# Performance work log

Hardware: AMD Instinct MI355X
Metric: run time of the kernel (lower is better)

The kernel has to match this reference:

```python
import jax, jax.numpy as jnp
import numpy as np

ALPHA = 1.0
GAMMA = 0.8
TAU = 0.1
NUM_SAMPLES = 10
TOP_K = 100
NUM_USER_GROUPS = 8
NUM_ITEM_GROUPS = 16
BATCH = 1024
NUM_ITEMS = 10000


def setup_inputs() -> dict:
    key = jax.random.key(0)
    k1, k2, k3, k4 = jax.random.split(key, 4)
    pred_scores = jax.random.normal(k1, (BATCH, NUM_ITEMS), dtype=jnp.float32)
    true_scores = jax.random.uniform(k2, (BATCH, NUM_ITEMS), dtype=jnp.float32)
    user_groups = jax.random.randint(k3, (BATCH,), 0, NUM_USER_GROUPS)
    item_groups = jax.random.randint(k4, (NUM_ITEMS,), 0, NUM_ITEM_GROUPS)
    return {
        "pred_scores": pred_scores,
        "true_scores": true_scores,
        "user_groups": user_groups,
        "item_groups": item_groups,
    }


def _calculate_exposure(scores):
    # scores: [B, k]. Soft-rank via Gumbel perturbations + pairwise sigmoid.
    B, k = scores.shape
    noise = jax.random.gumbel(jax.random.key(1), (NUM_SAMPLES, B, k), dtype=scores.dtype)
    noisy = scores[None, :, :] + noise                       # [S, B, k]
    diffs = noisy[..., :, None] - noisy[..., None, :]        # [S, B, k, k]
    # ranks = 1 + sum_j sigmoid((s_i - s_j)/tau) - sigmoid(0)
    ranks = 1.0 + jax.nn.sigmoid(diffs / TAU).sum(axis=-1) - 0.5  # [S, B, k]
    exposure = jnp.power(GAMMA, ranks - 1.0)                 # [S, B, k]
    return exposure.mean(axis=0)                             # [B, k]


def reference(pred_scores, true_scores, user_groups, item_groups):
    B = pred_scores.shape[0]
    # top-k selection (values == gathered pred scores)
    pred_topk, topk_idx = jax.lax.top_k(pred_scores, TOP_K)   # [B, k]
    item_groups_topk = item_groups[topk_idx]                  # [B, k]

    system_exposure = _calculate_exposure(pred_topk)          # [B, k]
    target_exposure = jnp.full_like(system_exposure, true_scores.mean())
    delta_E = system_exposure - target_exposure               # [B, k]

    ii_f_loss = jnp.mean(delta_E * delta_E)

    # group-pair scatter_mean
    pair_ids = user_groups[:, None] * NUM_ITEM_GROUPS + item_groups_topk  # [B, k]
    flat = delta_E.reshape(-1)
    pid = pair_ids.reshape(-1)
    num_pairs = NUM_USER_GROUPS * NUM_ITEM_GROUPS
    sums = jax.ops.segment_sum(flat, pid, num_segments=num_pairs)
    cnts = jax.ops.segment_sum(jnp.ones_like(flat), pid, num_segments=num_pairs)
    avg = jnp.where(cnts > 0, sums / jnp.maximum(cnts, 1.0), 0.0)
    gg_f_loss = jnp.mean(avg * avg)

    total_loss = ii_f_loss + ALPHA * gg_f_loss
    return (total_loss, ii_f_loss, gg_f_loss)
```

## Files before the change

kernel.cpp:

```cpp
#include <hip/hip_runtime.h>


typedef unsigned int u32;
typedef unsigned long long u64;

__device__ __forceinline__ u32 rotl32(u32 x, int r) { return (x << r) | (x >> (32 - r)); }

__device__ __forceinline__ void tf2x32(u32 k0, u32 k1, u32 x0, u32 x1, u32& o0, u32& o1) {
  u32 ks2 = 0x1BD11BDAu ^ k0 ^ k1;
#define TFR(r) { x0 += x1; x1 = rotl32(x1, r); x1 ^= x0; }
  x0 += k0; x1 += k1;
  TFR(13) TFR(15) TFR(26) TFR(6)
  x0 += k1; x1 += ks2 + 1u;
  TFR(17) TFR(29) TFR(16) TFR(24)
  x0 += ks2; x1 += k0 + 2u;
  TFR(13) TFR(15) TFR(26) TFR(6)
  x0 += k0; x1 += k1 + 3u;
  TFR(17) TFR(29) TFR(16) TFR(24)
  x0 += k1; x1 += ks2 + 4u;
  TFR(13) TFR(15) TFR(26) TFR(6)
  x0 += ks2; x1 += k0 + 5u;
#undef TFR
  o0 = x0; o1 = x1;
}

__device__ __forceinline__ float gumbel_noise(u32 i) {
  u32 o0, o1;
  tf2x32(0u, 1u, 0u, i, o0, o1);
  u32 bits = o0 ^ o1;
  float f = __uint_as_float((bits >> 9) | 0x3f800000u) - 1.0f;
  const float TINY = 1.17549435e-38f;
  float u = fmaxf(TINY, f + TINY);
  return -logf(-logf(u));
}

__device__ __forceinline__ u32 fkey(float v) {
  u32 u = __float_as_uint(v);
  return u ^ ((u & 0x80000000u) ? 0xFFFFFFFFu : 0x80000000u);
}

__device__ __forceinline__ void select_bin(const u32* __restrict__ hist, int shift,
                                           u32* sh_T, u32* sh_A, u32* sh_done,
                                           int lane) {
  u32 prevA = *sh_A;
  u32 target = 100u - prevA;
  u32 c0 = hist[lane * 4 + 0], c1 = hist[lane * 4 + 1];
  u32 c2 = hist[lane * 4 + 2], c3 = hist[lane * 4 + 3];
  u32 s = c0 + c1 + c2 + c3;
  u32 suf = s;
#pragma unroll
  for (int off = 1; off < 64; off <<= 1) {
    u32 o = __shfl_down(suf, off);
    suf += (lane + off < 64) ? o : 0u;
  }
  u32 sufx = suf - s;
  if (sufx < target && suf >= target) {
    u32 cc[4] = {c0, c1, c2, c3};
    u32 acc = sufx, bin = 0, cnt = 0;
#pragma unroll
    for (int k = 3; k >= 0; --k) {
      if (acc + cc[k] >= target) { bin = (u32)(lane * 4 + k); cnt = cc[k]; break; }
      acc += cc[k];
    }
    u32 newA = prevA + acc;
    *sh_T = *sh_T | (bin << shift);
    *sh_A = newA;
    *sh_done = (newA + cnt <= 128u || shift == 0) ? 1u : 0u;
  }
}

#define KSTAT 0xC0000000u

__global__ __launch_bounds__(512, 8) void selection_kernel(
    const float* __restrict__ pred,
    const float* __restrict__ ts,
    double* __restrict__ t_sum,
    u64* __restrict__ keyidx_ws) {
  const int N4 = 2500, K = 100;
  const int b = blockIdx.x;
  const int t = threadIdx.x;

  __shared__ u64 cand[2048];
  __shared__ u32 hist[256];
  __shared__ u64 sbuf[128];
  __shared__ u64 sorted[128];
  __shared__ u32 rankv[128];
  __shared__ float wred[8];
  __shared__ u32 sh_cnt, sh_nc, sh_T, sh_A, sh_done;

  if (t < 256) hist[t] = 0u;
  if (t < 128) rankv[t] = 0u;
  if (t == 0) { sh_cnt = 0u; sh_nc = 0u; sh_T = 0u; sh_A = 0u; sh_done = 0u; }
  __syncthreads();

  const float4* __restrict__ row4 = (const float4*)(pred + (size_t)b * 10000);
  const float4* __restrict__ tsr4 = (const float4*)(ts + (size_t)b * 10000);

  float tsum = 0.f;
#pragma unroll
  for (int k = 0; k < 5; ++k) {
    int i4 = t + (k << 9);
    if (k == 4 && i4 >= N4) break;
    float4 pp = row4[i4];
    float4 qq = tsr4[i4];
    tsum += (qq.x + qq.y) + (qq.z + qq.w);
#pragma unroll
    for (int c = 0; c < 4; ++c) {
      float v = (c == 0) ? pp.x : (c == 1) ? pp.y : (c == 2) ? pp.z : pp.w;
      u32 key = fkey(v);
      if (key >= KSTAT) {
        u32 pos = atomicAdd(&sh_cnt, 1u);
        int idx = i4 * 4 + c;
        if (pos < 2048u) cand[pos] = ((u64)key << 32) | (u32)(~(u32)idx);
      }
    }
  }
#pragma unroll
  for (int off = 32; off; off >>= 1) tsum += __shfl_down(tsum, off);
  if ((t & 63) == 0) wred[t >> 6] = tsum;
  __syncthreads();
  if (t == 0) {
    float s8 = 0.f;
#pragma unroll
    for (int w = 0; w < 8; ++w) s8 += wred[w];
    atomicAdd(t_sum, (double)s8);
  }

  u32 cnt_all = sh_cnt;
  bool fast = (cnt_all >= 100u && cnt_all <= 2048u);
  u32 nc = cnt_all < 2048u ? cnt_all : 2048u;

  if (fast) {
    for (int shift = 24; ; shift -= 8) {
      if (t < 256) hist[t] = 0u;
      __syncthreads();
      u32 pref = sh_T >> (shift + 8);
      for (int i = t; i < (int)nc; i += 512) {
        u32 key = (u32)(cand[i] >> 32);
        if (shift == 24 || (key >> (shift + 8)) == pref)
          atomicAdd(&hist[(key >> shift) & 255u], 1u);
      }
      __syncthreads();
      if (t < 64) select_bin(hist, shift, &sh_T, &sh_A, &sh_done, t);
      __syncthreads();
      if (sh_done) break;
    }
    u32 T = sh_T;
    for (int i = t; i < (int)nc; i += 512) {
      u64 p = cand[i];
      if ((u32)(p >> 32) >= T) {
        u32 pos = atomicAdd(&sh_nc, 1u);
        if (pos < 128u) sbuf[pos] = p;
      }
    }
  } else {
    for (int shift = 24; ; shift -= 8) {
      if (t < 256) hist[t] = 0u;
      __syncthreads();
      u32 pref = sh_T >> (shift + 8);
      for (int i4 = t; i4 < N4; i4 += 512) {
        float4 pp = row4[i4];
#pragma unroll
        for (int c = 0; c < 4; ++c) {
          float v = (c == 0) ? pp.x : (c == 1) ? pp.y : (c == 2) ? pp.z : pp.w;
          u32 key = fkey(v);
          if (shift == 24 || (key >> (shift + 8)) == pref)
            atomicAdd(&hist[(key >> shift) & 255u], 1u);
        }
      }
      __syncthreads();
      if (t < 64) select_bin(hist, shift, &sh_T, &sh_A, &sh_done, t);
      __syncthreads();
      if (sh_done) break;
    }
    u32 T = sh_T;
    for (int i4 = t; i4 < N4; i4 += 512) {
      float4 pp = row4[i4];
#pragma unroll
      for (int c = 0; c < 4; ++c) {
        float v = (c == 0) ? pp.x : (c == 1) ? pp.y : (c == 2) ? pp.z : pp.w;
        u32 key = fkey(v);
        if (key >= T) {
          u32 pos = atomicAdd(&sh_nc, 1u);
          int idx = i4 * 4 + c;
          if (pos < 128u) sbuf[pos] = ((u64)key << 32) | (u32)(~(u32)idx);
        }
      }
    }
  }
  __syncthreads();
  u32 nreal = sh_nc < 128u ? sh_nc : 128u;
  if (t < 128 && (u32)t >= nreal) sbuf[t] = 0ull;
  __syncthreads();

  {
    int e = t >> 2, seg = t & 3;
    u64 mykey = sbuf[e];
    u32 cnt = 0;
    int j0 = seg * 32;
#pragma unroll 8
    for (int j = j0; j < j0 + 32; ++j) cnt += (sbuf[j] > mykey) ? 1u : 0u;
    if (cnt) atomicAdd(&rankv[e], cnt);
    __syncthreads();
    if (t < 128) sorted[rankv[t]] = sbuf[t];
    __syncthreads();
  }

  if (t < K) keyidx_ws[(size_t)b * K + t] = sorted[t];
}

__global__ __launch_bounds__(512, 8) void expo_kernel(
    const u64* __restrict__ keyidx_ws,
    const int* __restrict__ ugrp, const int* __restrict__ igrp,
    double* __restrict__ sum_e, double* __restrict__ sum_e2,
    double* __restrict__ pair_sum, int* __restrict__ pair_cnt) {
  const int K = 100;
  const int b = blockIdx.x;
  const int t = threadIdx.x;

  __shared__ float topv[100];
  __shared__ int   pidv[100];
  __shared__ __align__(16) float noisy[1000];
  __shared__ float expo[100];
  __shared__ float pairS[128];
  __shared__ int   pairC[128];
  __shared__ float sh_bS, sh_bS2;

  if (t < 128) { pairS[t] = 0.f; pairC[t] = 0; }
  if (t < 100) expo[t] = 0.f;
  if (t == 0) { sh_bS = 0.f; sh_bS2 = 0.f; }
  int ug = ugrp[b];
  if (t < K) {
    u64 pk = keyidx_ws[(size_t)b * K + t];
    u32 key = (u32)(pk >> 32);
    u32 idx = ~(u32)pk;
    u32 u = (key & 0x80000000u) ? (key ^ 0x80000000u) : ~key;
    topv[t] = __uint_as_float(u);
    pidv[t] = ug * 16 + igrp[idx];
  }
  __syncthreads();

  for (int si = t; si < 1000; si += 512) {
    int s = si / 100, i = si - s * 100;
    noisy[si] = topv[i] + gumbel_noise(((u32)s * 1024u + (u32)b) * 100u + (u32)i);
  }
  __syncthreads();

  const float C2 = 14.426950408889634f;
  const float LG = -0.32192809488736235f;
  for (int si = t; si < 1000; si += 512) {
    int s = si / 100, i = si - s * 100;
    float nvC = noisy[si] * C2;
    const float4* nr4 = (const float4*)(noisy + s * 100);
    float S = 0.f;
#pragma unroll 5
    for (int jc = 0; jc < 25; ++jc) {
      float4 nj = nr4[jc];
      S += __builtin_amdgcn_rcpf(1.0f + exp2f(__builtin_fmaf(nj.x, C2, -nvC)));
      S += __builtin_amdgcn_rcpf(1.0f + exp2f(__builtin_fmaf(nj.y, C2, -nvC)));
      S += __builtin_amdgcn_rcpf(1.0f + exp2f(__builtin_fmaf(nj.z, C2, -nvC)));
      S += __builtin_amdgcn_rcpf(1.0f + exp2f(__builtin_fmaf(nj.w, C2, -nvC)));
    }
    float ex = exp2f((S - 0.5f) * LG);
    atomicAdd(&expo[i], ex);
  }
  __syncthreads();

  if (t < K) {
    float e = expo[t] * 0.1f;
    atomicAdd(&pairS[pidv[t]], e);
    atomicAdd(&pairC[pidv[t]], 1);
    atomicAdd(&sh_bS, e);
    atomicAdd(&sh_bS2, e * e);
  }
  __syncthreads();
  if (t < 128 && pairC[t] > 0) {
    atomicAdd(&pair_sum[t], (double)pairS[t]);
    atomicAdd(&pair_cnt[t], pairC[t]);
  }
  if (t == 0) {
    atomicAdd(sum_e, (double)sh_bS);
    atomicAdd(sum_e2, (double)sh_bS2);
  }
}

__global__ __launch_bounds__(128) void finalize_kernel(
    const double* __restrict__ t_sum, const double* __restrict__ sum_e,
    const double* __restrict__ sum_e2, const double* __restrict__ pair_sum,
    const int* __restrict__ pair_cnt, float* __restrict__ out) {
  int t = threadIdx.x;
  __shared__ double red[128];
  double tmean = *t_sum / 10240000.0;
  double g = 0.0;
  int c = pair_cnt[t];
  if (c > 0) {
    double avg = (pair_sum[t] - (double)c * tmean) / (double)c;
    g = avg * avg;
  }
  red[t] = g;
  __syncthreads();
#pragma unroll
  for (int off = 64; off; off >>= 1) {
    if (t < off) red[t] += red[t + off];
    __syncthreads();
  }
  if (t == 0) {
    double gg = red[0] / 128.0;
    double me = *sum_e / 102400.0;
    double me2 = *sum_e2 / 102400.0;
    double ii = me2 - 2.0 * tmean * me + tmean * tmean;
    out[0] = (float)(ii + gg);
    out[1] = (float)ii;
    out[2] = (float)gg;
  }
}

extern "C" void kernel_launch(void* const* d_in, const int* in_sizes, int n_in,
                              void* d_out, int out_size, void* d_ws, size_t ws_size,
                              hipStream_t stream) {
  (void)in_sizes; (void)n_in; (void)out_size; (void)ws_size;
  const float* pred = (const float*)d_in[0];
  const float* ts   = (const float*)d_in[1];
  const int*   ugrp = (const int*)d_in[2];
  const int*   igrp = (const int*)d_in[3];
  float* out = (float*)d_out;

  double* t_sum    = (double*)d_ws;
  double* sum_e    = t_sum + 1;
  double* sum_e2   = t_sum + 2;
  double* pair_sum = t_sum + 3;
  int*    pair_cnt = (int*)(t_sum + 3 + 128);
  u64*    keyidx   = (u64*)((char*)d_ws + (3 + 128) * sizeof(double) + 128 * sizeof(int));

  hipMemsetAsync(d_ws, 0, (3 + 128) * sizeof(double) + 128 * sizeof(int), stream);

  selection_kernel<<<1024, 512, 0, stream>>>(pred, ts, t_sum, keyidx);
  expo_kernel<<<1024, 512, 0, stream>>>(keyidx, ugrp, igrp,
                                        sum_e, sum_e2, pair_sum, pair_cnt);
  finalize_kernel<<<1, 128, 0, stream>>>(t_sum, sum_e, sum_e2, pair_sum, pair_cnt, out);
}
```

Before: 168.3 us.

## Exploit sigmoid antisymmetry to halve pairwise exp work in exposure kernel

Uses sigmoid(x)+sigmoid(-x)=1 so each thread computes only half of the pairwise sigmoids, over a circular window of 49 or 50 neighbours. The complementary contributions are scattered to the partner rows through shared-memory atomicAdds into a new SP buffer, and a constant offset recovers the rank. Noisy scores are pre-scaled and stored with a wraparound copy to avoid modulo indexing. This halves the exp/rcp transcendental work but adds a shared atomic per pair, which may contend and cost more than it saves.

```diff
diff --git a/kernel.cpp b/kernel.cpp
--- a/kernel.cpp
+++ b/kernel.cpp
@@ -220,15 +220,23 @@
 
   __shared__ float topv[100];
   __shared__ int   pidv[100];
-  __shared__ __align__(16) float noisy[1000];
+  __shared__ float nC[10][152];
+  __shared__ float SP[10][100];
   __shared__ float expo[100];
   __shared__ float pairS[128];
   __shared__ int   pairC[128];
   __shared__ float sh_bS, sh_bS2;
 
+  const float C2 = 14.426950408889634f;
+  const float LG = -0.32192809488736235f;
+
   if (t < 128) { pairS[t] = 0.f; pairC[t] = 0; }
   if (t < 100) expo[t] = 0.f;
   if (t == 0) { sh_bS = 0.f; sh_bS2 = 0.f; }
+  for (int si = t; si < 1000; si += 512) {
+    int s = si / 100, i = si - s * 100;
+    SP[s][i] = 0.f;
+  }
   int ug = ugrp[b];
   if (t < K) {
     u64 pk = keyidx_ws[(size_t)b * K + t];
@@ -242,26 +250,38 @@
 
   for (int si = t; si < 1000; si += 512) {
     int s = si / 100, i = si - s * 100;
-    noisy[si] = topv[i] + gumbel_noise(((u32)s * 1024u + (u32)b) * 100u + (u32)i);
-  }
-  __syncthreads();
-
-  const float C2 = 14.426950408889634f;
-  const float LG = -0.32192809488736235f;
+    float nvc = (topv[i] + gumbel_noise(((u32)s * 1024u + (u32)b) * 100u + (u32)i)) * C2;
+    nC[s][i] = nvc;
+    if (i < 50) nC[s][i + 100] = nvc;
+  }
+  __syncthreads();
+
   for (int si = t; si < 1000; si += 512) {
     int s = si / 100, i = si - s * 100;
-    float nvC = noisy[si] * C2;
-    const float4* nr4 = (const float4*)(noisy + s * 100);
-    float S = 0.f;
-#pragma unroll 5
-    for (int jc = 0; jc < 25; ++jc) {
-      float4 nj = nr4[jc];
-      S += __builtin_amdgcn_rcpf(1.0f + exp2f(__builtin_fmaf(nj.x, C2, -nvC)));
-      S += __builtin_amdgcn_rcpf(1.0f + exp2f(__builtin_fmaf(nj.y, C2, -nvC)));
-      S += __builtin_amdgcn_rcpf(1.0f + exp2f(__builtin_fmaf(nj.z, C2, -nvC)));
-      S += __builtin_amdgcn_rcpf(1.0f + exp2f(__builtin_fmaf(nj.w, C2, -nvC)));
-    }
-    float ex = exp2f((S - 0.5f) * LG);
+    const float* nrow = &nC[s][0];
+    float* sprow = &SP[s][0];
+    float niC = nrow[i];
+    float own0 = 0.f, own1 = 0.f;
+#pragma unroll 7
+    for (int k = 1; k <= 49; ++k) {
+      float sig = __builtin_amdgcn_rcpf(1.0f + exp2f(nrow[i + k] - niC));
+      if (k & 1) own0 += sig; else own1 += sig;
+      int jj = i + k; if (jj >= 100) jj -= 100;
+      atomicAdd(&sprow[jj], -sig);
+    }
+    if (i < 50) {
+      float sig = __builtin_amdgcn_rcpf(1.0f + exp2f(nrow[i + 50] - niC));
+      own0 += sig;
+      atomicAdd(&sprow[i + 50], -sig);
+    }
+    atomicAdd(&sprow[i], own0 + own1);
+  }
+  __syncthreads();
+
+  for (int si = t; si < 1000; si += 512) {
+    int s = si / 100, i = si - s * 100;
+    float rank_m1 = SP[s][i] + 49.0f + (i >= 50 ? 1.0f : 0.0f);
+    float ex = exp2f(rank_m1 * LG);
     atomicAdd(&expo[i], ex);
   }
   __syncthreads();
```

Result: slower. 392.4 us (+133.2%).
